# Kernel optimization log

Hardware: AMD Instinct MI355X
Metric: run time of the kernel (lower is better)

Reference implementation:

```python
import jax, jax.numpy as jnp
import numpy as np

N, E, B = 50000, 800000, 128
NF, ED, HID, HEADS, DH, OUT, L = 7, 2, 128, 4, 32, 64, 3
EPS = 1e-5
NEG_SLOPE = 0.2


def _layer_norm(x, g, b):
    mu = jnp.mean(x, axis=-1, keepdims=True)
    v = jnp.mean((x - mu) ** 2, axis=-1, keepdims=True)
    return g * (x - mu) / jnp.sqrt(v + EPS) + b


def setup_inputs() -> dict:
    key = jax.random.key(0)
    ks = jax.random.split(key, 32)
    s = 0.05
    inp = {
        "x": jax.random.normal(ks[0], (N, NF), jnp.float32),
        "edge_index": jax.random.randint(ks[1], (2, E), 0, N, jnp.int32),
        "edge_attr": jax.random.uniform(ks[2], (E, ED), jnp.float32),
        "batch": jnp.sort(jax.random.randint(ks[3], (N,), 0, B, jnp.int32)),
        # node encoder
        "enc_W": jax.random.normal(ks[4], (NF, HID)) * (1.0 / np.sqrt(NF)),
        "enc_b": jnp.zeros((HID,)),
        "enc_g": jnp.ones((HID,)),
        "enc_bb": jnp.zeros((HID,)),
        # GATv2 layers (stacked over L)
        "gat_Wsrc": jax.random.normal(ks[5], (L, HID, HID)) * (1.0 / np.sqrt(HID)),
        "gat_Wdst": jax.random.normal(ks[6], (L, HID, HID)) * (1.0 / np.sqrt(HID)),
        "gat_We": jax.random.normal(ks[7], (L, ED, HID)) * (1.0 / np.sqrt(ED)),
        "gat_att": jax.random.normal(ks[8], (L, HEADS, DH)) * s,
        "gat_bias": jnp.zeros((L, HID)),
        # GraphNorm per layer
        "gn_w": jnp.ones((L, HID)),
        "gn_b": jnp.zeros((L, HID)),
        "gn_s": jnp.ones((L, HID)),  # mean_scale
        # attention pooling
        "pool_W1": jax.random.normal(ks[9], (HID, HID)) * (1.0 / np.sqrt(HID)),
        "pool_b1": jnp.zeros((HID,)),
        "pool_W2": jax.random.normal(ks[10], (HID, 1)) * (1.0 / np.sqrt(HID)),
        # output mapper
        "map_W1": jax.random.normal(ks[11], (HID, HID)) * (1.0 / np.sqrt(HID)),
        "map_b1": jnp.zeros((HID,)),
        "map_g": jnp.ones((HID,)),
        "map_bb": jnp.zeros((HID,)),
        "map_W2": jax.random.normal(ks[12], (HID, OUT)) * (1.0 / np.sqrt(HID)),
        "map_b2": jnp.zeros((OUT,)),
    }
    return inp


def _segment_softmax(scores, seg, num_seg):
    # scores: [E2, HEADS], seg: [E2] destination node ids
    m = jax.ops.segment_max(scores, seg, num_segments=num_seg)
    ex = jnp.exp(scores - m[seg])
    denom = jax.ops.segment_sum(ex, seg, num_segments=num_seg)
    return ex / denom[seg]


def _gatv2(x, src, dst, ea, Wsrc, Wdst, We, att, bias):
    e2 = src.shape[0]
    xl = (x @ Wsrc)[src].reshape(e2, HEADS, DH)   # lin_l(x_j), source
    xr = (x @ Wdst)[dst].reshape(e2, HEADS, DH)   # lin_r(x_i), target
    ee = (ea @ We).reshape(e2, HEADS, DH)
    z = jax.nn.leaky_relu(xl + xr + ee, NEG_SLOPE)
    score = jnp.einsum("ehd,hd->eh", z, att)
    alpha = _segment_softmax(score, dst, N)       # softmax over incoming edges
    msg = (xl * alpha[:, :, None]).reshape(e2, HID)
    out = jax.ops.segment_sum(msg, dst, num_segments=N)
    return out + bias


def _graph_norm(x, batch, w, b, scale):
    cnt = jax.ops.segment_sum(jnp.ones((N,), x.dtype), batch, num_segments=B)
    cnt = jnp.maximum(cnt, 1.0)[:, None]
    mean = jax.ops.segment_sum(x, batch, num_segments=B) / cnt
    xc = x - scale * mean[batch]
    var = jax.ops.segment_sum(xc * xc, batch, num_segments=B) / cnt
    return w * xc / jnp.sqrt(var[batch] + EPS) + b


def reference(x, edge_index, edge_attr, batch, enc_W, enc_b, enc_g, enc_bb,
              gat_Wsrc, gat_Wdst, gat_We, gat_att, gat_bias, gn_w, gn_b, gn_s,
              pool_W1, pool_b1, pool_W2, map_W1, map_b1, map_g, map_bb,
              map_W2, map_b2):
    # node encoder: Linear -> ReLU -> LayerNorm
    h = _layer_norm(jax.nn.relu(x @ enc_W + enc_b), enc_g, enc_bb)

    # add self loops; self-loop edge_attr = mean of edge_attr (PyG fill_value='mean')
    loop = jnp.arange(N, dtype=edge_index.dtype)
    src = jnp.concatenate([edge_index[0], loop])
    dst = jnp.concatenate([edge_index[1], loop])
    ea_mean = jnp.mean(edge_attr, axis=0)
    ea = jnp.concatenate([edge_attr, jnp.broadcast_to(ea_mean, (N, ED))], axis=0)

    for i in range(L):
        out = _gatv2(h, src, dst, ea, gat_Wsrc[i], gat_Wdst[i], gat_We[i],
                     gat_att[i], gat_bias[i])
        out = out + h  # residual (in_dim == out_dim -> Identity proj)
        out = _graph_norm(out, batch, gn_w[i], gn_b[i], gn_s[i])
        h = jax.nn.elu(out)

    node_emb = h
    # attention pooling: softmax over ALL nodes (dim=0, as in source)
    scores = jnp.tanh(h @ pool_W1 + pool_b1) @ pool_W2          # [N, 1]
    weights = jax.nn.softmax(scores, axis=0)
    g = jax.ops.segment_sum(h * weights, batch, num_segments=B)  # [B, HID]

    # output mapper (dropout inactive at eval)
    g = _layer_norm(jax.nn.relu(g @ map_W1 + map_b1), map_g, map_bb)
    graph_emb = g @ map_W2 + map_b2
    return graph_emb, node_emb
```

## Files before the change

### kernel.cpp

```cpp
#include <hip/hip_runtime.h>
#include <hip/hip_bf16.h>

typedef __hip_bfloat16 bf16;
typedef __attribute__((ext_vector_type(8))) short short8;
typedef __attribute__((ext_vector_type(4))) float float4v;
typedef float f32x2 __attribute__((ext_vector_type(2)));

#define Nn   50000
#define Ee   800000
#define E2   850000
#define Bb   128
#define NFd  7
#define HID  128
#define OUTD 64
#define EPS  1e-5f
#define SLOPE 0.2f
#define LOG2E 1.4426950408889634f
#define NSTRIP 3125
#define NPAIR  1563

#define MFMA16(a,b,c) __builtin_amdgcn_mfma_f32_16x16x32_bf16(a,b,c,0,0,0)

__device__ __forceinline__ float lane_bcast(float v, int l){
  return __int_as_float(__builtin_amdgcn_readlane(__float_as_int(v), l));
}
__device__ __forceinline__ float wred_sum(float v){
  #pragma unroll
  for (int o=32;o;o>>=1) v += __shfl_xor(v, o, 64);
  return v;
}
#define UPD_DPP(x, ctrl) \
  __int_as_float(__builtin_amdgcn_update_dpp(0, __float_as_int(x), (ctrl), 0xf, 0xf, false))
__device__ __forceinline__ float red4_quad(float x){
  x = x + UPD_DPP(x, 0xB1);
  x = x + UPD_DPP(x, 0x4E);
  return x;
}
__device__ __forceinline__ unsigned fkey(float f){
  unsigned u = __float_as_uint(f);
  return (u & 0x80000000u) ? ~u : (u | 0x80000000u);
}
__device__ __forceinline__ float fkeyinv(unsigned k){
  unsigned u = (k & 0x80000000u) ? (k ^ 0x80000000u) : ~k;
  return __uint_as_float(u);
}
__device__ __forceinline__ float tanh_fast(float x){
  float e = __expf(fminf(fmaxf(2.f*x, -30.f), 30.f));
  return (e-1.f)/(e+1.f);
}
__device__ __forceinline__ float bf_lo(unsigned u){ return __uint_as_float(u<<16); }
__device__ __forceinline__ float bf_hi(unsigned u){ return __uint_as_float(u & 0xffff0000u); }
__device__ __forceinline__ unsigned short f2bs(float f){
  bf16 h = __float2bfloat16(f);
  return *reinterpret_cast<unsigned short*>(&h);
}
__device__ __forceinline__ unsigned pack2(float a, float b){
  return (unsigned)f2bs(a) | ((unsigned)f2bs(b) << 16);
}
__device__ __forceinline__ int xcd_swizzle(int bid, int nwg){
  int q = nwg >> 3, r = nwg & 7;
  int x = bid & 7, i = bid >> 3;
  return (x < r ? x*(q+1) : r*(q+1) + (x-r)*q) + i;
}

__global__ __launch_bounds__(256) void k_wprep(
    const float* __restrict__ gWsrc, const float* __restrict__ gWdst,
    const float* __restrict__ pW1,
    unsigned* __restrict__ wtimg, unsigned* __restrict__ pw1img){
  int idx = blockIdx.x*256 + threadIdx.x;
  if (idx < 3*256*64){
    int l  = idx / (256*64);
    int r  = idx - l*(256*64);
    int n  = r >> 6;
    int kp = r & 63;
    const float* Wp = (n < 128) ? (gWsrc + (size_t)l*HID*HID)
                                : (gWdst + (size_t)l*HID*HID - 128);
    float w0 = Wp[(2*kp)*HID + n];
    float w1 = Wp[(2*kp+1)*HID + n];
    int byt = (n*256 + kp*4) ^ ((n&7)<<4);
    *(unsigned*)((char*)(wtimg + (size_t)l*16384) + byt) = pack2(w0, w1);
  } else {
    int r = idx - 3*256*64;
    if (r < 128*64){
      int n  = r >> 6;
      int kp = r & 63;
      float w0 = pW1[(2*kp)*HID + n];
      float w1 = pW1[(2*kp+1)*HID + n];
      int byt = (n*256 + kp*4) ^ ((n&7)<<4);
      *(unsigned*)((char*)pw1img + byt) = pack2(w0, w1);
    }
  }
}

__global__ __launch_bounds__(256) void k_encoder(
    const float* __restrict__ x, const float* __restrict__ W, const float* __restrict__ b,
    const float* __restrict__ g, const float* __restrict__ bbv,
    unsigned* __restrict__ hbu){
  int wv = (blockIdx.x*blockDim.x + threadIdx.x) >> 6;
  if (wv >= Nn) return;
  int lane = threadIdx.x & 63;
  int d0 = 2*lane, d1 = d0+1;
  float y0 = b[d0], y1 = b[d1];
  #pragma unroll
  for (int i=0;i<NFd;++i){
    float xv = x[wv*NFd + i];
    y0 = fmaf(xv, W[i*HID + d0], y0);
    y1 = fmaf(xv, W[i*HID + d1], y1);
  }
  y0 = fmaxf(y0, 0.f); y1 = fmaxf(y1, 0.f);
  float mu = wred_sum(y0+y1) * (1.f/HID);
  float c0 = y0-mu, c1 = y1-mu;
  float var = wred_sum(c0*c0 + c1*c1) * (1.f/HID);
  float rs = rsqrtf(var + EPS);
  float v0 = g[d0]*c0*rs + bbv[d0];
  float v1 = g[d1]*c1*rs + bbv[d1];
  hbu[(size_t)wv*64 + lane] = pack2(v0, v1);
}

__global__ void k_ea_deg(const int* __restrict__ ei, const float* __restrict__ ea,
    int* __restrict__ deg, float* __restrict__ eam){
  int tid = blockIdx.x*blockDim.x + threadIdx.x;
  const float2* ea2 = (const float2*)ea;
  float a0=0.f, a1=0.f;
  for (int e=tid; e<Ee; e += gridDim.x*blockDim.x){
    float2 v = ea2[e];
    a0 += v.x; a1 += v.y;
    atomicAdd(&deg[ei[Ee + e]], 1);
  }
  a0 = wred_sum(a0); a1 = wred_sum(a1);
  if ((threadIdx.x & 63)==0){
    atomicAdd(&eam[0], a0*(1.f/Ee));
    atomicAdd(&eam[1], a1*(1.f/Ee));
  }
}

__global__ __launch_bounds__(1024) void k_scan(const int* __restrict__ deg,
    int* __restrict__ offs, int* __restrict__ cursor){
  __shared__ int wsum[16];
  __shared__ int tot_s;
  __shared__ int carry_s;
  int t = threadIdx.x, lane = t & 63, wid = t >> 6;
  if (t==0) carry_s = 0;
  __syncthreads();
  for (int base=0; base<Nn; base += 4096){
    int i0 = base + t*4;
    int v0=0,v1=0,v2=0,v3=0;
    if (i0+3 < Nn){
      int4 qv = *(const int4*)(deg + i0);
      v0=qv.x+1; v1=qv.y+1; v2=qv.z+1; v3=qv.w+1;
    } else {
      if (i0   < Nn) v0 = deg[i0]+1;
      if (i0+1 < Nn) v1 = deg[i0+1]+1;
      if (i0+2 < Nn) v2 = deg[i0+2]+1;
      if (i0+3 < Nn) v3 = deg[i0+3]+1;
    }
    int tot = v0+v1+v2+v3;
    int x = tot;
    #pragma unroll
    for (int o=1;o<64;o<<=1){ int u = __shfl_up(x, o, 64); if (lane >= o) x += u; }
    if (lane==63) wsum[wid] = x;
    __syncthreads();
    if (t==0){ int s=0; for (int k=0;k<16;++k){ int tv=wsum[k]; wsum[k]=s; s+=tv; } tot_s = s; }
    __syncthreads();
    int excl = carry_s + wsum[wid] + (x - tot);
    int p0 = excl, p1 = excl+v0, p2 = p1+v1, p3 = p2+v2;
    if (i0+3 < Nn){
      *(int4*)(offs + i0)   = make_int4(p0,p1,p2,p3);
      *(int4*)(cursor + i0) = make_int4(p0,p1,p2,p3);
    } else {
      if (i0   < Nn){ offs[i0]  =p0; cursor[i0]  =p0; }
      if (i0+1 < Nn){ offs[i0+1]=p1; cursor[i0+1]=p1; }
      if (i0+2 < Nn){ offs[i0+2]=p2; cursor[i0+2]=p2; }
      if (i0+3 < Nn){ offs[i0+3]=p3; cursor[i0+3]=p3; }
    }
    __syncthreads();
    if (t==0) carry_s += tot_s;
    __syncthreads();
  }
  if (t==0) offs[Nn] = carry_s;
}

__global__ void k_scatter(const int* __restrict__ ei, const float* __restrict__ ea,
    const float* __restrict__ eam, int* __restrict__ cursor,
    int4* __restrict__ ecomb){
  int e = blockIdx.x*blockDim.x + threadIdx.x;
  if (e >= E2 + 16) return;
  if (e >= E2){
    ecomb[e] = make_int4(0, 0, 0, 0);
    return;
  }
  int s, d; float a0, a1;
  if (e < Ee){
    s = ei[e]; d = ei[Ee + e];
    float2 v = ((const float2*)ea)[e];
    a0 = v.x; a1 = v.y;
  } else {
    s = d = e - Ee; a0 = eam[0]; a1 = eam[1];
  }
  int pos = atomicAdd(&cursor[d], 1);
  ecomb[pos] = make_int4(s, __float_as_int(a0), __float_as_int(a1), 0);
}

__global__ void k_gstart(const int* __restrict__ batch, int* __restrict__ gstart){
  int n = blockIdx.x*blockDim.x + threadIdx.x;
  if (n >= Nn) return;
  int bc = batch[n];
  int bp = (n==0) ? -1 : batch[n-1];
  for (int b = bp+1; b <= bc; ++b) gstart[b] = n;
  if (n == Nn-1){ for (int b = bc+1; b <= Bb; ++b) gstart[b] = Nn; }
}

__global__ __launch_bounds__(256) void k_dualgemm(
    const unsigned* __restrict__ hbu, const unsigned* __restrict__ wtimg,
    unsigned* __restrict__ hsb, float* __restrict__ hd){
  __shared__ unsigned wt[16384];
  for (int i = threadIdx.x; i < 4096; i += 256)
    ((uint4*)wt)[i] = ((const uint4*)wtimg)[i];
  __syncthreads();
  int wid = threadIdx.x >> 6, lane = threadIdx.x & 63;
  int q = lane >> 4, c = lane & 15;
  const unsigned short* hb = (const unsigned short*)hbu;
  for (int pr = blockIdx.x*4 + wid; pr < NPAIR; pr += gridDim.x*4){
    int p0 = 2*pr, p1 = 2*pr + 1;
    bool v1 = (p1 < NSTRIP);
    int node0 = p0*16 + c;
    int node1 = v1 ? (p1*16 + c) : node0;
    short8 bf0[4], bf1[4];
    const unsigned short* hp0 = hb + (size_t)node0*HID + q*8;
    const unsigned short* hp1 = hb + (size_t)node1*HID + q*8;
    #pragma unroll
    for (int s=0;s<4;++s){
      bf0[s] = *(const short8*)(hp0 + s*32);
      bf1[s] = *(const short8*)(hp1 + s*32);
    }
    #pragma unroll 4
    for (int t=0;t<16;++t){
      float4v ac0 = {0.f,0.f,0.f,0.f}, ac1 = {0.f,0.f,0.f,0.f};
      #pragma unroll
      for (int s=0;s<4;++s){
        int row = t*16 + c;
        int byt = (row*256 + s*64 + q*16) ^ ((row&7)<<4);
        short8 af = *(const short8*)((const char*)wt + byt);
        ac0 = MFMA16(af, bf0[s], ac0);
        ac1 = MFMA16(af, bf1[s], ac1);
      }
      if (t < 8){
        int co = t*8 + q*2;
        *(uint2*)(hsb + (size_t)node0*64 + co) =
            make_uint2(pack2(ac0[0],ac0[1]), pack2(ac0[2],ac0[3]));
        if (v1) *(uint2*)(hsb + (size_t)node1*64 + co) =
            make_uint2(pack2(ac1[0],ac1[1]), pack2(ac1[2],ac1[3]));
      } else {
        int dd = (t-8)*16 + q*4;
        *(float4*)(hd + (size_t)node0*HID + dd) = make_float4(ac0[0],ac0[1],ac0[2],ac0[3]);
        if (v1) *(float4*)(hd + (size_t)node1*HID + dd) = make_float4(ac1[0],ac1[1],ac1[2],ac1[3]);
      }
    }
  }
}

__global__ __launch_bounds__(256) void k_edge(const unsigned* __restrict__ hsb,
    float* __restrict__ hdio, const unsigned* __restrict__ hbu,
    const int4* __restrict__ ecomb,
    const int* __restrict__ offs, const float* __restrict__ We,
    const float* __restrict__ att, const float* __restrict__ bias){
  int bid = xcd_swizzle(blockIdx.x, gridDim.x);
  int n = (bid*256 + (int)threadIdx.x) >> 6;
  if (n >= Nn) return;
  int lane = threadIdx.x & 63;
  int row = lane >> 4;
  int c   = lane & 15;
  int d0  = 8*c;
  f32x2 we0v[4], we1v[4], atv[4], xrv[4];
  #pragma unroll
  for (int k=0;k<4;++k){
    we0v[k] = *(const f32x2*)(We + d0 + 2*k);
    we1v[k] = *(const f32x2*)(We + HID + d0 + 2*k);
    f32x2 a = *(const f32x2*)(att + d0 + 2*k);
    atv[k]  = a * LOG2E;
    xrv[k]  = *(const f32x2*)(hdio + (size_t)n*HID + d0 + 2*k);
  }
  int e0 = offs[n], e1 = offs[n+1];
  float m = 0.f, ssum = 0.f;
  f32x2 accv[4];
  #pragma unroll
  for (int k=0;k<4;++k) accv[k] = (f32x2){0.f,0.f};

  int4  r0 = ecomb[e0 + row];
  uint4 x0 = *(const uint4*)(hsb + ((size_t)(unsigned)r0.x<<6) + 4*c);
  int4  r1 = ecomb[e0 + 4 + row];
  uint4 x1 = *(const uint4*)(hsb + ((size_t)(unsigned)r1.x<<6) + 4*c);
  for (int e = e0; e < e1; e += 4){
    int4  r2 = ecomb[e + 8 + row];
    uint4 x2 = *(const uint4*)(hsb + ((size_t)(unsigned)r2.x<<6) + 4*c);
    bool vC = (e + row) < e1;
    f32x2 xl2[4];
    xl2[0] = (f32x2){bf_lo(x0.x), bf_hi(x0.x)};
    xl2[1] = (f32x2){bf_lo(x0.y), bf_hi(x0.y)};
    xl2[2] = (f32x2){bf_lo(x0.z), bf_hi(x0.z)};
    xl2[3] = (f32x2){bf_lo(x0.w), bf_hi(x0.w)};
    float ex = __int_as_float(r0.y), ey = __int_as_float(r0.z);
    f32x2 ex2 = (f32x2){ex, ex};
    f32x2 ey2 = (f32x2){ey, ey};
    f32x2 dotv = (f32x2){0.f, 0.f};
    #pragma unroll
    for (int k=0;k<4;++k){
      f32x2 z = __builtin_elementwise_fma(ey2, we1v[k],
                  __builtin_elementwise_fma(ex2, we0v[k], xl2[k] + xrv[k]));
      z = __builtin_elementwise_max(z, z * SLOPE);
      dotv = __builtin_elementwise_fma(z, atv[k], dotv);
    }
    float sc = red4_quad(dotv.x + dotv.y);
    if (e == e0) m = __shfl(sc, lane & 15, 64);
    float p = exp2f(sc - m);
    p = vC ? p : 0.f;
    ssum += p;
    f32x2 pv = (f32x2){p, p};
    #pragma unroll
    for (int k=0;k<4;++k) accv[k] = __builtin_elementwise_fma(pv, xl2[k], accv[k]);
    r0=r1; x0=x1; r1=r2; x1=x2;
  }
  float acc[8];
  #pragma unroll
  for (int k=0;k<4;++k){ acc[2*k] = accv[k].x; acc[2*k+1] = accv[k].y; }
  #pragma unroll
  for (int j=0;j<8;++j){
    acc[j] += __shfl_xor(acc[j], 16, 64);
    acc[j] += __shfl_xor(acc[j], 32, 64);
  }
  ssum += __shfl_xor(ssum, 16, 64);
  ssum += __shfl_xor(ssum, 32, 64);
  if (row == 0){
    float inv = 1.f/ssum;
    uint4 hu = *(const uint4*)(hbu + ((size_t)n<<6) + 4*c);
    float hr[8];
    hr[0]=bf_lo(hu.x); hr[1]=bf_hi(hu.x); hr[2]=bf_lo(hu.y); hr[3]=bf_hi(hu.y);
    hr[4]=bf_lo(hu.z); hr[5]=bf_hi(hu.z); hr[6]=bf_lo(hu.w); hr[7]=bf_hi(hu.w);
    float o[8];
    #pragma unroll
    for (int j=0;j<8;++j) o[j] = fmaf(acc[j], inv, bias[d0+j] + hr[j]);
    *(float4*)(hdio + (size_t)n*HID + d0)     = make_float4(o[0],o[1],o[2],o[3]);
    *(float4*)(hdio + (size_t)n*HID + d0 + 4) = make_float4(o[4],o[5],o[6],o[7]);
  }
}

__global__ __launch_bounds__(128) void k_gn_reduce(const float* __restrict__ out,
    const int* __restrict__ gstart, float* __restrict__ gsum_, float* __restrict__ gsq_){
  int b = blockIdx.x >> 4, sub = blockIdx.x & 15;
  int ns = gstart[b], ne = gstart[b+1];
  int d = threadIdx.x;
  float s = 0.f, qq = 0.f;
  for (int n = ns + sub; n < ne; n += 16){
    float v = out[(size_t)n*HID + d];
    s += v; qq = fmaf(v, v, qq);
  }
  atomicAdd(&gsum_[b*HID + d], s);
  atomicAdd(&gsq_[b*HID + d], qq);
}

__global__ __launch_bounds__(256) void k_gn_apply(const float* __restrict__ out,
    const float* __restrict__ gsum_, const float* __restrict__ gsq_,
    const int* __restrict__ gstart, const int* __restrict__ batch,
    const float* __restrict__ gw, const float* __restrict__ gb,
    const float* __restrict__ gs,
    unsigned* __restrict__ hbu, float* __restrict__ emb){
  int n = (blockIdx.x*blockDim.x + threadIdx.x) >> 6;
  if (n >= Nn) return;
  int lane = threadIdx.x & 63;
  int b = batch[n];
  float icnt = 1.f / fmaxf((float)(gstart[b+1]-gstart[b]), 1.f);
  int d0 = 2*lane, d1 = d0+1;
  float2 x = *(const float2*)(out + (size_t)n*HID + d0);
  float mean0 = gsum_[b*HID+d0]*icnt, mean1 = gsum_[b*HID+d1]*icnt;
  float ms0 = mean0*gs[d0], ms1 = mean1*gs[d1];
  float var0 = gsq_[b*HID+d0]*icnt - ms0*(2.f*mean0 - ms0);
  float var1 = gsq_[b*HID+d1]*icnt - ms1*(2.f*mean1 - ms1);
  float rs0 = rsqrtf(fmaxf(var0, 0.f) + EPS);
  float rs1 = rsqrtf(fmaxf(var1, 0.f) + EPS);
  float y0 = gw[d0]*(x.x - ms0)*rs0 + gb[d0];
  float y1 = gw[d1]*(x.y - ms1)*rs1 + gb[d1];
  y0 = (y0 > 0.f) ? y0 : (__expf(y0) - 1.f);
  y1 = (y1 > 0.f) ? y1 : (__expf(y1) - 1.f);
  hbu[(size_t)n*64 + lane] = pack2(y0, y1);
  if (emb) *(float2*)(emb + (size_t)n*HID + d0) = make_float2(y0, y1);
}

__global__ __launch_bounds__(256) void k_pool_score(
    const unsigned* __restrict__ hbu, const unsigned* __restrict__ pw1img,
    const float* __restrict__ b1, const float* __restrict__ W2,
    float* __restrict__ score, unsigned* __restrict__ mkey){
  __shared__ unsigned wt[8192];
  __shared__ float b1l[HID], w2l[HID];
  for (int i = threadIdx.x; i < 2048; i += 256)
    ((uint4*)wt)[i] = ((const uint4*)pw1img)[i];
  if (threadIdx.x < HID){ b1l[threadIdx.x] = b1[threadIdx.x]; w2l[threadIdx.x] = W2[threadIdx.x]; }
  __syncthreads();
  int wid = threadIdx.x >> 6, lane = threadIdx.x & 63;
  int q = lane >> 4, c = lane & 15;
  const unsigned short* hb = (const unsigned short*)hbu;
  float bmax = -1e30f;
  for (int p = blockIdx.x*4 + wid; p < NSTRIP; p += gridDim.x*4){
    int node = p*16 + c;
    short8 bf[4];
    const unsigned short* hp = hb + (size_t)node*HID + q*8;
    #pragma unroll
    for (int s=0;s<4;++s) bf[s] = *(const short8*)(hp + s*32);
    float part = 0.f;
    #pragma unroll
    for (int t=0;t<8;++t){
      float4v ac = {0.f,0.f,0.f,0.f};
      #pragma unroll
      for (int s=0;s<4;++s){
        int row = t*16 + c;
        int byt = (row*256 + s*64 + q*16) ^ ((row&7)<<4);
        ac = MFMA16(*(const short8*)((const char*)wt + byt), bf[s], ac);
      }
      int dim = t*16 + q*4;
      #pragma unroll
      for (int r=0;r<4;++r)
        part += tanh_fast(ac[r] + b1l[dim+r]) * w2l[dim+r];
    }
    part += __shfl_xor(part, 16, 64);
    part += __shfl_xor(part, 32, 64);
    if (q==0) score[node] = part;
    bmax = fmaxf(bmax, part);
  }
  #pragma unroll
  for (int o=32;o;o>>=1) bmax = fmaxf(bmax, __shfl_xor(bmax, o, 64));
  if (lane==0) atomicMax(mkey, fkey(bmax));
}

__global__ __launch_bounds__(128) void k_pool_reduce(const unsigned* __restrict__ hbu,
    const float* __restrict__ score, const unsigned* __restrict__ mkey,
    const int* __restrict__ gstart, float* __restrict__ gsum, float* __restrict__ total){
  int b = blockIdx.x >> 4, sub = blockIdx.x & 15;
  int ns = gstart[b], ne = gstart[b+1];
  float mx = fkeyinv(*mkey);
  int d = threadIdx.x;
  float acc = 0.f, es = 0.f;
  for (int n = ns + sub; n < ne; n += 16){
    float ev = __expf(score[n] - mx);
    unsigned u = hbu[(size_t)n*64 + (d>>1)];
    float hv = (d & 1) ? bf_hi(u) : bf_lo(u);
    acc = fmaf(ev, hv, acc);
    if (d==0) es += ev;
  }
  atomicAdd(&gsum[b*HID + d], acc);
  if (d==0) atomicAdd(total, es);
}

__global__ __launch_bounds__(64) void k_mapper(const float* __restrict__ gsum,
    const float* __restrict__ total,
    const float* __restrict__ W1, const float* __restrict__ b1,
    const float* __restrict__ g,  const float* __restrict__ bbv,
    const float* __restrict__ W2, const float* __restrict__ b2v,
    float* __restrict__ out0){
  int b = blockIdx.x, lane = threadIdx.x;
  float inv = 1.f/(*total);
  int d0 = 2*lane, d1 = d0+1;
  float gv0 = gsum[b*HID + d0]*inv, gv1 = gsum[b*HID + d1]*inv;
  float a0 = b1[d0], a1 = b1[d1];
  for (int i=0;i<HID;++i){
    float hv = lane_bcast((i&1) ? gv1 : gv0, i>>1);
    a0 = fmaf(hv, W1[i*HID + d0], a0);
    a1 = fmaf(hv, W1[i*HID + d1], a1);
  }
  a0 = fmaxf(a0, 0.f); a1 = fmaxf(a1, 0.f);
  float mu = wred_sum(a0+a1) * (1.f/HID);
  float c0 = a0-mu, c1 = a1-mu;
  float var = wred_sum(c0*c0 + c1*c1) * (1.f/HID);
  float rs = rsqrtf(var + EPS);
  float l0 = g[d0]*c0*rs + bbv[d0];
  float l1 = g[d1]*c1*rs + bbv[d1];
  float acc = b2v[lane];
  for (int j=0;j<HID;++j){
    float lv = lane_bcast((j&1) ? l1 : l0, j>>1);
    acc = fmaf(lv, W2[j*OUTD + lane], acc);
  }
  out0[b*OUTD + lane] = acc;
}

extern "C" void kernel_launch(void* const* d_in, const int* in_sizes, int n_in,
                              void* d_out, int out_size, void* d_ws, size_t ws_size,
                              hipStream_t stream){
  const float* x     = (const float*)d_in[0];
  const int*   ei    = (const int*)  d_in[1];
  const float* ea    = (const float*)d_in[2];
  const int*   batch = (const int*)  d_in[3];
  const float* encW  = (const float*)d_in[4];
  const float* encb  = (const float*)d_in[5];
  const float* encg  = (const float*)d_in[6];
  const float* encbb = (const float*)d_in[7];
  const float* gWsrc = (const float*)d_in[8];
  const float* gWdst = (const float*)d_in[9];
  const float* gWe   = (const float*)d_in[10];
  const float* gatt  = (const float*)d_in[11];
  const float* gbias = (const float*)d_in[12];
  const float* gnw   = (const float*)d_in[13];
  const float* gnb   = (const float*)d_in[14];
  const float* gns   = (const float*)d_in[15];
  const float* pW1   = (const float*)d_in[16];
  const float* pb1   = (const float*)d_in[17];
  const float* pW2   = (const float*)d_in[18];
  const float* mW1   = (const float*)d_in[19];
  const float* mb1   = (const float*)d_in[20];
  const float* mg    = (const float*)d_in[21];
  const float* mbb   = (const float*)d_in[22];
  const float* mW2   = (const float*)d_in[23];
  const float* mb2   = (const float*)d_in[24];

  char* w = (char*)d_ws;
  size_t off = 0;
  auto alloc = [&](size_t bytes)->char*{
    char* p = w + off;
    off += (bytes + 255) & ~(size_t)255;
    return p;
  };
  unsigned* hbu    = (unsigned*)alloc((size_t)Nn*64*4);
  unsigned* hsb    = (unsigned*)alloc((size_t)Nn*64*4);
  float*    hd     = (float*)   alloc((size_t)Nn*HID*4);
  int4*     ecomb  = (int4*)    alloc((size_t)(E2+16)*16);
  int*      offs   = (int*)     alloc((size_t)(Nn+1)*4);
  int*      cursor = (int*)     alloc((size_t)Nn*4);
  int*      deg    = (int*)     alloc((size_t)Nn*4);
  int*      gstart = (int*)     alloc((size_t)(Bb+1)*4);
  float*    score  = (float*)   alloc((size_t)Nn*4);
  float*    gsum   = (float*)   alloc((size_t)Bb*HID*4 * 7);
  float*    gnbase = gsum + Bb*HID;
  unsigned* wtimg  = (unsigned*)alloc((size_t)3*16384*4);
  unsigned* pw1img = (unsigned*)alloc((size_t)8192*4);
  float*    scal   = (float*)   alloc(256);
  float*    eam   = scal;
  float*    total = scal + 2;
  unsigned* mkey  = (unsigned*)(scal + 3);

  float* out_graph = (float*)d_out;
  float* out_node  = (float*)d_out + (size_t)Bb*OUTD;

  hipMemsetAsync(deg,  0, (size_t)Nn*4, stream);
  hipMemsetAsync(scal, 0, 256, stream);
  hipMemsetAsync(gsum, 0, (size_t)Bb*HID*4 * 7, stream);

  k_wprep<<<224, 256, 0, stream>>>(gWsrc, gWdst, pW1, wtimg, pw1img);
  k_encoder<<<Nn/4, 256, 0, stream>>>(x, encW, encb, encg, encbb, hbu);
  k_ea_deg<<<1024, 256, 0, stream>>>(ei, ea, deg, eam);
  k_scan<<<1, 1024, 0, stream>>>(deg, offs, cursor);
  k_scatter<<<(E2+16+255)/256, 256, 0, stream>>>(ei, ea, eam, cursor, ecomb);
  k_gstart<<<(Nn+255)/256, 256, 0, stream>>>(batch, gstart);

  for (int l = 0; l < 3; ++l){
    float* gnsum_l = gnbase + (size_t)l*2*Bb*HID;
    float* gnsq_l  = gnsum_l + Bb*HID;
    k_dualgemm<<<392, 256, 0, stream>>>(hbu, wtimg + (size_t)l*16384, hsb, hd);
    k_edge<<<Nn/4, 256, 0, stream>>>(hsb, hd, hbu, ecomb, offs,
                                     gWe + (size_t)l*2*HID,
                                     gatt + (size_t)l*4*32,
                                     gbias + (size_t)l*HID);
    k_gn_reduce<<<Bb*16, 128, 0, stream>>>(hd, gstart, gnsum_l, gnsq_l);
    k_gn_apply<<<Nn/4, 256, 0, stream>>>(hd, gnsum_l, gnsq_l, gstart, batch,
                                         gnw + (size_t)l*HID, gnb + (size_t)l*HID,
                                         gns + (size_t)l*HID, hbu,
                                         (l==2) ? out_node : (float*)nullptr);
  }

  k_pool_score<<<256, 256, 0, stream>>>(hbu, pw1img, pb1, pW2, score, mkey);
  k_pool_reduce<<<Bb*16, 128, 0, stream>>>(hbu, score, mkey, gstart, gsum, total);
  k_mapper<<<Bb, 64, 0, stream>>>(gsum, total, mW1, mb1, mg, mbb, mW2, mb2, out_graph);
}
```

Measured before the change: 610.8 us.

## Split degree counting from edge-attr mean and de-vectorize edge loop with shallower prefetch

New measurement: 538.9 us, median of 2. 11.8% less time.

```diff
diff --git a/kernel.cpp b/kernel.cpp
--- a/kernel.cpp
+++ b/kernel.cpp
@@ -4,7 +4,6 @@
 typedef __hip_bfloat16 bf16;
 typedef __attribute__((ext_vector_type(8))) short short8;
 typedef __attribute__((ext_vector_type(4))) float float4v;
-typedef float f32x2 __attribute__((ext_vector_type(2)));
 
 #define Nn   50000
 #define Ee   800000
@@ -117,21 +116,25 @@
   hbu[(size_t)wv*64 + lane] = pack2(v0, v1);
 }
 
-__global__ void k_ea_deg(const int* __restrict__ ei, const float* __restrict__ ea,
-    int* __restrict__ deg, float* __restrict__ eam){
+__global__ void k_ea_mean(const float* __restrict__ ea, float* __restrict__ eam){
   int tid = blockIdx.x*blockDim.x + threadIdx.x;
   const float2* ea2 = (const float2*)ea;
   float a0=0.f, a1=0.f;
   for (int e=tid; e<Ee; e += gridDim.x*blockDim.x){
     float2 v = ea2[e];
     a0 += v.x; a1 += v.y;
-    atomicAdd(&deg[ei[Ee + e]], 1);
   }
   a0 = wred_sum(a0); a1 = wred_sum(a1);
   if ((threadIdx.x & 63)==0){
     atomicAdd(&eam[0], a0*(1.f/Ee));
     atomicAdd(&eam[1], a1*(1.f/Ee));
   }
+}
+
+__global__ void k_deg(const int* __restrict__ ei, int* __restrict__ deg){
+  int e = blockIdx.x*blockDim.x + threadIdx.x;
+  if (e >= Ee) return;
+  atomicAdd(&deg[ei[Ee + e]], 1);
 }
 
 __global__ __launch_bounds__(1024) void k_scan(const int* __restrict__ deg,
@@ -271,58 +274,49 @@
   int row = lane >> 4;
   int c   = lane & 15;
   int d0  = 8*c;
-  f32x2 we0v[4], we1v[4], atv[4], xrv[4];
+  float we0[8], we1[8], at[8], xr[8];
   #pragma unroll
-  for (int k=0;k<4;++k){
-    we0v[k] = *(const f32x2*)(We + d0 + 2*k);
-    we1v[k] = *(const f32x2*)(We + HID + d0 + 2*k);
-    f32x2 a = *(const f32x2*)(att + d0 + 2*k);
-    atv[k]  = a * LOG2E;
-    xrv[k]  = *(const f32x2*)(hdio + (size_t)n*HID + d0 + 2*k);
-  }
+  for (int j=0;j<8;++j){
+    we0[j] = We[d0+j];
+    we1[j] = We[HID+d0+j];
+    at[j]  = att[d0+j] * LOG2E;
+  }
+  *(float4*)(xr)   = *(const float4*)(hdio + (size_t)n*HID + d0);
+  *(float4*)(xr+4) = *(const float4*)(hdio + (size_t)n*HID + d0 + 4);
   int e0 = offs[n], e1 = offs[n+1];
   float m = 0.f, ssum = 0.f;
-  f32x2 accv[4];
+  float acc[8];
   #pragma unroll
-  for (int k=0;k<4;++k) accv[k] = (f32x2){0.f,0.f};
-
-  int4  r0 = ecomb[e0 + row];
-  uint4 x0 = *(const uint4*)(hsb + ((size_t)(unsigned)r0.x<<6) + 4*c);
-  int4  r1 = ecomb[e0 + 4 + row];
-  uint4 x1 = *(const uint4*)(hsb + ((size_t)(unsigned)r1.x<<6) + 4*c);
+  for (int j=0;j<8;++j) acc[j] = 0.f;
+
+  int4  rC = ecomb[e0 + row];
+  uint4 xC = *(const uint4*)(hsb + ((size_t)(unsigned)rC.x<<6) + 4*c);
+  bool  vC = (e0 + row) < e1;
   for (int e = e0; e < e1; e += 4){
-    int4  r2 = ecomb[e + 8 + row];
-    uint4 x2 = *(const uint4*)(hsb + ((size_t)(unsigned)r2.x<<6) + 4*c);
-    bool vC = (e + row) < e1;
-    f32x2 xl2[4];
-    xl2[0] = (f32x2){bf_lo(x0.x), bf_hi(x0.x)};
-    xl2[1] = (f32x2){bf_lo(x0.y), bf_hi(x0.y)};
-    xl2[2] = (f32x2){bf_lo(x0.z), bf_hi(x0.z)};
-    xl2[3] = (f32x2){bf_lo(x0.w), bf_hi(x0.w)};
-    float ex = __int_as_float(r0.y), ey = __int_as_float(r0.z);
-    f32x2 ex2 = (f32x2){ex, ex};
-    f32x2 ey2 = (f32x2){ey, ey};
-    f32x2 dotv = (f32x2){0.f, 0.f};
-    #pragma unroll
-    for (int k=0;k<4;++k){
-      f32x2 z = __builtin_elementwise_fma(ey2, we1v[k],
-                  __builtin_elementwise_fma(ex2, we0v[k], xl2[k] + xrv[k]));
-      z = __builtin_elementwise_max(z, z * SLOPE);
-      dotv = __builtin_elementwise_fma(z, atv[k], dotv);
-    }
-    float sc = red4_quad(dotv.x + dotv.y);
+    int en = e + 4 + row;
+    int4  rN = ecomb[en];
+    uint4 xN = *(const uint4*)(hsb + ((size_t)(unsigned)rN.x<<6) + 4*c);
+    bool  vN = en < e1;
+    float xl[8];
+    xl[0]=bf_lo(xC.x); xl[1]=bf_hi(xC.x); xl[2]=bf_lo(xC.y); xl[3]=bf_hi(xC.y);
+    xl[4]=bf_lo(xC.z); xl[5]=bf_hi(xC.z); xl[6]=bf_lo(xC.w); xl[7]=bf_hi(xC.w);
+    float eCx = __int_as_float(rC.y), eCy = __int_as_float(rC.z);
+    float dot = 0.f;
+    #pragma unroll
+    for (int j=0;j<8;++j){
+      float z = fmaf(eCy, we1[j], fmaf(eCx, we0[j], xl[j] + xr[j]));
+      z = fmaxf(z, SLOPE*z);
+      dot = fmaf(z, at[j], dot);
+    }
+    float sc = red4_quad(dot);
     if (e == e0) m = __shfl(sc, lane & 15, 64);
     float p = exp2f(sc - m);
     p = vC ? p : 0.f;
     ssum += p;
-    f32x2 pv = (f32x2){p, p};
-    #pragma unroll
-    for (int k=0;k<4;++k) accv[k] = __builtin_elementwise_fma(pv, xl2[k], accv[k]);
-    r0=r1; x0=x1; r1=r2; x1=x2;
-  }
-  float acc[8];
-  #pragma unroll
-  for (int k=0;k<4;++k){ acc[2*k] = accv[k].x; acc[2*k+1] = accv[k].y; }
+    #pragma unroll
+    for (int j=0;j<8;++j) acc[j] = fmaf(p, xl[j], acc[j]);
+    rC=rN; xC=xN; vC=vN;
+  }
   #pragma unroll
   for (int j=0;j<8;++j){
     acc[j] += __shfl_xor(acc[j], 16, 64);
@@ -543,7 +537,8 @@
 
   k_wprep<<<224, 256, 0, stream>>>(gWsrc, gWdst, pW1, wtimg, pw1img);
   k_encoder<<<Nn/4, 256, 0, stream>>>(x, encW, encb, encg, encbb, hbu);
-  k_ea_deg<<<1024, 256, 0, stream>>>(ei, ea, deg, eam);
+  k_ea_mean<<<256, 256, 0, stream>>>(ea, eam);
+  k_deg<<<(Ee+255)/256, 256, 0, stream>>>(ei, deg);
   k_scan<<<1, 1024, 0, stream>>>(deg, offs, cursor);
   k_scatter<<<(E2+16+255)/256, 256, 0, stream>>>(ei, ea, eam, cursor, ecomb);
   k_gstart<<<(Nn+255)/256, 256, 0, stream>>>(batch, gstart);
```
